# Optimization experiments

Measured on AMD Instinct MI355X. Metric: run time of the kernel, lower is better.

The kernel has to match this reference:

```python
import jax, jax.numpy as jnp
import numpy as np

B, N, C, H = 4, 2048, 256, 8
D = C // H  # head_dim = 32


def setup_inputs() -> dict:
    key = jax.random.key(0)
    ks = jax.random.split(key, 6)
    scale = 0.02
    return {
        "x": jax.random.normal(ks[0], (B, N, C), dtype=jnp.float32),
        # PPI interaction strengths in [0,1] (buffer, not trained)
        "interaction_mask": jax.random.uniform(ks[1], (N, N), dtype=jnp.float32),
        "W_qkv": jax.random.normal(ks[2], (C, 3 * C), dtype=jnp.float32) * scale,
        "b_qkv": jnp.zeros((3 * C,), dtype=jnp.float32),
        "W_out": jax.random.normal(ks[3], (C, C), dtype=jnp.float32) * scale,
        "b_out": jnp.zeros((C,), dtype=jnp.float32),
    }


def reference(x, interaction_mask, W_qkv, b_qkv, W_out, b_out):
    Bb, Nn, Cc = x.shape
    scale = D ** -0.5
    qkv = (x @ W_qkv + b_qkv).reshape(Bb, Nn, 3, H, D)
    qkv = jnp.transpose(qkv, (2, 0, 3, 1, 4))  # [3, B, H, N, D]
    q, k, v = qkv[0], qkv[1], qkv[2]
    # scores [B, H, N, N], modulated pre-softmax by biological mask
    attn = jnp.einsum("bhnd,bhmd->bhnm", q, k) * scale
    attn = attn * (0.1 + 0.9 * interaction_mask)[None, None, :, :]
    attn = jax.nn.softmax(attn, axis=-1)  # dropout is identity in eval
    out = jnp.einsum("bhnm,bhmd->bhnd", attn, v)
    out = jnp.transpose(out, (0, 2, 1, 3)).reshape(Bb, Nn, Cc)
    return out @ W_out + b_out
```

## Files before the change

kernel.cpp:

```cpp
#include <hip/hip_runtime.h>
#include <hip/hip_bf16.h>

#define B_ 4
#define N_ 2048
#define C_ 256
#define H_ 8
#define D_ 32

typedef __attribute__((ext_vector_type(4))) short bf16x4;
typedef __attribute__((ext_vector_type(8))) short bf16x8;
typedef __attribute__((ext_vector_type(16))) float f32x16;

static __device__ __forceinline__ float b2f(short u) {
    unsigned v = ((unsigned)(unsigned short)u) << 16;
    return __builtin_bit_cast(float, v);
}
static __device__ __forceinline__ short f2bs(float f) {
    __hip_bfloat16 h = __float2bfloat16(f);
    return __builtin_bit_cast(short, h);
}


__global__ __launch_bounds__(256) void x_relayout(const float* __restrict__ x,
                                                  short* __restrict__ xF) {
    const int idx = blockIdx.x * 256 + threadIdx.x;
    const int row = idx >> 6, c0 = (idx & 63) * 4;
    const float4 f4 = *(const float4*)(x + (size_t)row * 256 + c0);
    const int mt = row >> 5, l5 = row & 31;
    const int kt = c0 >> 5, dd0 = c0 & 31;
    const int hi = (dd0 >> 2) & 1, s0 = 4 * (dd0 >> 3);
    bf16x4 o;
    o[0] = f2bs(f4.x); o[1] = f2bs(f4.y); o[2] = f2bs(f4.z); o[3] = f2bs(f4.w);
    *(bf16x4*)(xF + (((size_t)mt * 8 + kt) * 32 + l5) * 32 + hi * 16 + s0) = o;
}

__global__ __launch_bounds__(256) void w_relayout(const float* __restrict__ Wq,
                                                  const float* __restrict__ Wo,
                                                  short* __restrict__ wqF,
                                                  short* __restrict__ woF) {
    int idx = blockIdx.x * 256 + threadIdx.x;
    const float* W; short* dst; int ncols;
    if (idx < 49152) { W = Wq; dst = wqF; ncols = 768; }
    else { idx -= 49152; W = Wo; dst = woF; ncols = 256; }
    const int f4pr = ncols >> 2;
    const int row = idx / f4pr, c0 = (idx % f4pr) * 4;
    const float4 f4 = *(const float4*)(W + (size_t)row * ncols + c0);
    const int kt = row >> 5, dd = row & 31;
    const int hi = (dd >> 2) & 1, s = (dd & 3) + 4 * (dd >> 3);
    const float vals[4] = {f4.x, f4.y, f4.z, f4.w};
#pragma unroll
    for (int j = 0; j < 4; ++j) {
        const int col = c0 + j, nt = col >> 5, l5 = col & 31;
        dst[(((size_t)nt * 8 + kt) * 32 + l5) * 32 + hi * 16 + s] = f2bs(vals[j]);
    }
}

__global__ __launch_bounds__(256) void mask_relayout(const float* __restrict__ mask,
                                                     short* __restrict__ maskF) {
    const int t = threadIdx.x;
    const int n = blockIdx.y * 64 + (t & 63);
    const int mt = blockIdx.x * 4 + (t >> 6);
    const float cf = 0.17677669529663687f * 1.4426950408889634f;
    float v[32];
    const float4* src = (const float4*)(mask + (size_t)n * N_ + mt * 32);
#pragma unroll
    for (int i = 0; i < 8; ++i) {
        const float4 f4 = src[i];
        v[i * 4 + 0] = f4.x; v[i * 4 + 1] = f4.y;
        v[i * 4 + 2] = f4.z; v[i * 4 + 3] = f4.w;
    }
#pragma unroll
    for (int hi = 0; hi < 2; ++hi) {
        bf16x8 o0, o1;
#pragma unroll
        for (int r = 0; r < 16; ++r) {
            const int crow = (r & 3) + 8 * (r >> 2) + 4 * hi;
            const short s = f2bs(cf * (0.1f + 0.9f * v[crow]));
            if (r < 8) o0[r] = s; else o1[r - 8] = s;
        }
        short* dst = maskF + ((size_t)(mt * 2 + hi) * N_ + n) * 16;
        *(bf16x8*)dst = o0;
        *(bf16x8*)(dst + 8) = o1;
    }
}

__global__ __launch_bounds__(256, 4) void qkv_mfma(const short* __restrict__ xF,
                                                   const short* __restrict__ wqF,
                                                   const float* __restrict__ bias,
                                                   short* __restrict__ qb,
                                                   short* __restrict__ kbF,
                                                   short* __restrict__ vbF) {
    __shared__ short sc[4][32 * 34];
    const int t = threadIdx.x;
    const int w = t >> 6, lane = t & 63, l5 = lane & 31, hi = lane >> 5;
    const int tile = blockIdx.x * 4 + w;
    const int nt = tile % 24, mt = tile / 24;
    f32x16 acc;
#pragma unroll
    for (int i = 0; i < 16; ++i) acc[i] = 0.f;
    const short* ap = xF + ((size_t)mt * 8 * 32) * 32 + l5 * 32 + hi * 16;
    const short* bp = wqF + ((size_t)nt * 8 * 32) * 32 + l5 * 32 + hi * 16;
#pragma unroll
    for (int kt = 0; kt < 8; ++kt) {
        const bf16x8 a0 = *(const bf16x8*)(ap + kt * 1024);
        const bf16x8 a1 = *(const bf16x8*)(ap + kt * 1024 + 8);
        const bf16x8 b0 = *(const bf16x8*)(bp + kt * 1024);
        const bf16x8 b1 = *(const bf16x8*)(bp + kt * 1024 + 8);
        acc = __builtin_amdgcn_mfma_f32_32x32x16_bf16(a0, b0, acc, 0, 0, 0);
        acc = __builtin_amdgcn_mfma_f32_32x32x16_bf16(a1, b1, acc, 0, 0, 0);
    }
    const float bq = bias[nt * 32 + l5];
    short* myc = sc[w];
#pragma unroll
    for (int r = 0; r < 16; ++r)
        myc[((r & 3) + 8 * (r >> 2) + 4 * hi) * 34 + l5] = f2bs(acc[r] + bq);
    __syncthreads();

    const int h = nt & 7, t3 = nt >> 3;
    const int mtk = mt & 63;
    const size_t bh = (size_t)(mt >> 6) * 8 + h;
    if (t3 == 0) {
        const bf16x8 r0 = *(const bf16x8*)(myc + l5 * 34 + hi * 16);
        const bf16x8 r1 = *(const bf16x8*)(myc + l5 * 34 + hi * 16 + 8);
        short* dst = qb + (bh * N_ + (size_t)mtk * 32 + l5) * D_ + hi * 16;
        *(bf16x8*)dst = r0;
        *(bf16x8*)(dst + 8) = r1;
    } else if (t3 == 1) {
        bf16x8 o0, o1;
#pragma unroll
        for (int s = 0; s < 16; ++s) {
            const int dd = hi * 4 + (s & 3) + 8 * (s >> 2);
            const short vv = myc[l5 * 34 + dd];
            if (s < 8) o0[s] = vv; else o1[s - 8] = vv;
        }
        short* dst = kbF + ((bh * 64 + mtk) * 32 + l5) * 32 + hi * 16;
        *(bf16x8*)dst = o0;
        *(bf16x8*)(dst + 8) = o1;
    } else {
        bf16x8 o0, o1;
#pragma unroll
        for (int s = 0; s < 16; ++s) {
            const int nl = hi * 4 + (s & 3) + 8 * (s >> 2);
            const short vv = myc[nl * 34 + l5];
            if (s < 8) o0[s] = vv; else o1[s - 8] = vv;
        }
        short* dst = vbF + ((bh * 64 + mtk) * 32 + l5) * 32 + hi * 16;
        *(bf16x8*)dst = o0;
        *(bf16x8*)(dst + 8) = o1;
    }
}

__global__ __launch_bounds__(256, 4) void attn_mfma(const short* __restrict__ qb,
                                                    const short* __restrict__ kbF,
                                                    const short* __restrict__ vbF,
                                                    const short* __restrict__ maskF,
                                                    short* __restrict__ aoF) {
    __shared__ float red[4][32][33];
    __shared__ float Ls[4][32];
    const int t = threadIdx.x;
    const int w = t >> 6, lane = t & 63, l5 = lane & 31, hi = lane >> 5;
    const int hi4 = hi * 4;
    const int bh = blockIdx.x >> 5, qg = blockIdx.x & 31;
    const int q0 = qg * 64;
    const int nqA = q0 + l5, nqB = q0 + 32 + l5;

    const short* qrA = qb + ((size_t)bh * N_ + nqA) * D_;
    const short* qrB = qb + ((size_t)bh * N_ + nqB) * D_;
    const bf16x8 qfA0 = __builtin_shufflevector(*(const bf16x4*)(qrA + hi4),
                                                *(const bf16x4*)(qrA + hi4 + 8),
                                                0, 1, 2, 3, 4, 5, 6, 7);
    const bf16x8 qfA1 = __builtin_shufflevector(*(const bf16x4*)(qrA + hi4 + 16),
                                                *(const bf16x4*)(qrA + hi4 + 24),
                                                0, 1, 2, 3, 4, 5, 6, 7);
    const bf16x8 qfB0 = __builtin_shufflevector(*(const bf16x4*)(qrB + hi4),
                                                *(const bf16x4*)(qrB + hi4 + 8),
                                                0, 1, 2, 3, 4, 5, 6, 7);
    const bf16x8 qfB1 = __builtin_shufflevector(*(const bf16x4*)(qrB + hi4 + 16),
                                                *(const bf16x4*)(qrB + hi4 + 24),
                                                0, 1, 2, 3, 4, 5, 6, 7);
    f32x16 accA, accB;
#pragma unroll
    for (int i = 0; i < 16; ++i) { accA[i] = 0.f; accB[i] = 0.f; }
    float lsA = 0.f, lsB = 0.f;

    const size_t fragbase = (size_t)bh * 64 * 1024;
#pragma unroll 4
    for (int i = 0; i < 16; ++i) {
        const int mt = w * 16 + i;
        const short* kp = kbF + fragbase + (size_t)mt * 1024 + l5 * 32 + hi * 16;
        const bf16x8 af0 = *(const bf16x8*)kp;
        const bf16x8 af1 = *(const bf16x8*)(kp + 8);
        f32x16 sA, sB;
#pragma unroll
        for (int j = 0; j < 16; ++j) { sA[j] = 0.f; sB[j] = 0.f; }
        sA = __builtin_amdgcn_mfma_f32_32x32x16_bf16(af0, qfA0, sA, 0, 0, 0);
        sA = __builtin_amdgcn_mfma_f32_32x32x16_bf16(af1, qfA1, sA, 0, 0, 0);
        sB = __builtin_amdgcn_mfma_f32_32x32x16_bf16(af0, qfB0, sB, 0, 0, 0);
        sB = __builtin_amdgcn_mfma_f32_32x32x16_bf16(af1, qfB1, sB, 0, 0, 0);

        const short* mpA = maskF + ((size_t)(mt * 2 + hi) * N_ + nqA) * 16;
        const short* mpB = maskF + ((size_t)(mt * 2 + hi) * N_ + nqB) * 16;
        const bf16x8 mA0 = *(const bf16x8*)mpA;
        const bf16x8 mA1 = *(const bf16x8*)(mpA + 8);
        const bf16x8 mB0 = *(const bf16x8*)mpB;
        const bf16x8 mB1 = *(const bf16x8*)(mpB + 8);

        bf16x8 pfA0, pfA1, pfB0, pfB1;
#pragma unroll
        for (int r = 0; r < 16; ++r) {
            const float fmA = b2f(r < 8 ? mA0[r] : mA1[r - 8]);
            const float fmB = b2f(r < 8 ? mB0[r] : mB1[r - 8]);
            const float pA = __builtin_amdgcn_exp2f(sA[r] * fmA);
            const float pB = __builtin_amdgcn_exp2f(sB[r] * fmB);
            lsA += pA; lsB += pB;
            const short hA = f2bs(pA), hB = f2bs(pB);
            if (r < 8) { pfA0[r] = hA; pfB0[r] = hB; }
            else       { pfA1[r - 8] = hA; pfB1[r - 8] = hB; }
        }
        const short* vp = vbF + fragbase + (size_t)mt * 1024 + l5 * 32 + hi * 16;
        const bf16x8 vf0 = *(const bf16x8*)vp;
        const bf16x8 vf1 = *(const bf16x8*)(vp + 8);
        accA = __builtin_amdgcn_mfma_f32_32x32x16_bf16(vf0, pfA0, accA, 0, 0, 0);
        accA = __builtin_amdgcn_mfma_f32_32x32x16_bf16(vf1, pfA1, accA, 0, 0, 0);
        accB = __builtin_amdgcn_mfma_f32_32x32x16_bf16(vf0, pfB0, accB, 0, 0, 0);
        accB = __builtin_amdgcn_mfma_f32_32x32x16_bf16(vf1, pfB1, accB, 0, 0, 0);
    }

    const int h = bh & 7;
    const int gmtb = (bh >> 3) * 64 + qg * 2;
#pragma unroll
    for (int tq = 0; tq < 2; ++tq) {
        if (tq) __syncthreads();
        const float lsum = tq ? lsB : lsA;
        const f32x16 acc = tq ? accB : accA;
        const float lt = lsum + __shfl_xor(lsum, 32);
        Ls[w][l5] = lt;
#pragma unroll
        for (int r = 0; r < 16; ++r)
            red[w][(r & 3) + 8 * (r >> 2) + hi4][l5] = acc[r];
        __syncthreads();
        const int row = t & 31, hi2 = (t >> 5) & 1, sh = t >> 6;
        const float inv = 1.0f / (Ls[0][row] + Ls[1][row] + Ls[2][row] + Ls[3][row]);
        bf16x4 o;
#pragma unroll
        for (int j = 0; j < 4; ++j) {
            const int dd = hi2 * 4 + j + 8 * sh;
            o[j] = f2bs((red[0][dd][row] + red[1][dd][row] +
                         red[2][dd][row] + red[3][dd][row]) * inv);
        }
        const size_t gmt = gmtb + tq;
        *(bf16x4*)(aoF + ((gmt * 8 + h) * 32 + row) * 32 + hi2 * 16 + sh * 4) = o;
    }
}

__global__ __launch_bounds__(256, 4) void out_mfma(const short* __restrict__ aoF,
                                                   const short* __restrict__ woF,
                                                   const float* __restrict__ bias,
                                                   float* __restrict__ out) {
    const int t = threadIdx.x;
    const int w = t >> 6, lane = t & 63, l5 = lane & 31, hi = lane >> 5;
    const int tile = blockIdx.x * 4 + w;
    const int nt = tile & 7, mt = tile >> 3;
    f32x16 acc;
#pragma unroll
    for (int i = 0; i < 16; ++i) acc[i] = 0.f;
    const short* ap = aoF + (size_t)mt * 8192 + l5 * 32 + hi * 16;
    const short* bp = woF + (size_t)nt * 8192 + l5 * 32 + hi * 16;
#pragma unroll
    for (int kt = 0; kt < 8; ++kt) {
        const bf16x8 a0 = *(const bf16x8*)(ap + kt * 1024);
        const bf16x8 a1 = *(const bf16x8*)(ap + kt * 1024 + 8);
        const bf16x8 b0 = *(const bf16x8*)(bp + kt * 1024);
        const bf16x8 b1 = *(const bf16x8*)(bp + kt * 1024 + 8);
        acc = __builtin_amdgcn_mfma_f32_32x32x16_bf16(a0, b0, acc, 0, 0, 0);
        acc = __builtin_amdgcn_mfma_f32_32x32x16_bf16(a1, b1, acc, 0, 0, 0);
    }
    const float bo = bias[nt * 32 + l5];
#pragma unroll
    for (int r = 0; r < 16; ++r) {
        const int crow = (r & 3) + 8 * (r >> 2) + 4 * hi;
        out[(size_t)(mt * 32 + crow) * 256 + nt * 32 + l5] = acc[r] + bo;
    }
}

extern "C" void kernel_launch(void* const* d_in, const int* in_sizes, int n_in,
                              void* d_out, int out_size, void* d_ws, size_t ws_size,
                              hipStream_t stream) {
    const float* x = (const float*)d_in[0];
    const float* mask = (const float*)d_in[1];
    const float* W_qkv = (const float*)d_in[2];
    const float* b_qkv = (const float*)d_in[3];
    const float* W_out = (const float*)d_in[4];
    const float* b_out = (const float*)d_in[5];
    float* out = (float*)d_out;

    const size_t per = (size_t)B_ * H_ * N_ * D_;
    short* qb = (short*)d_ws;
    short* kbF = qb + per;
    short* vbF = kbF + per;
    short* maskF = vbF + per;
    short* xF = maskF + (size_t)N_ * N_;
    short* wqF = xF + per;
    short* woF = wqF + 196608;
    short* aoF = xF;

    x_relayout<<<2048, 256, 0, stream>>>(x, xF);
    w_relayout<<<256, 256, 0, stream>>>(W_qkv, W_out, wqF, woF);
    mask_relayout<<<dim3(16, 32), 256, 0, stream>>>(mask, maskF);
    qkv_mfma<<<1536, 256, 0, stream>>>(xF, wqF, b_qkv, qb, kbF, vbF);
    attn_mfma<<<1024, 256, 0, stream>>>(qb, kbF, vbF, maskF, aoF);
    out_mfma<<<512, 256, 0, stream>>>(aoF, woF, b_out, out);
}
```

Measured before the change: 79.48 us.

## Merge relayout kernels, split MFMA accumulators, reorder attention loads, remap blocks

```diff
diff --git a/kernel.cpp b/kernel.cpp
--- a/kernel.cpp
+++ b/kernel.cpp
@@ -21,66 +21,69 @@
 }
 
 
-__global__ __launch_bounds__(256) void x_relayout(const float* __restrict__ x,
-                                                  short* __restrict__ xF) {
-    const int idx = blockIdx.x * 256 + threadIdx.x;
-    const int row = idx >> 6, c0 = (idx & 63) * 4;
-    const float4 f4 = *(const float4*)(x + (size_t)row * 256 + c0);
-    const int mt = row >> 5, l5 = row & 31;
-    const int kt = c0 >> 5, dd0 = c0 & 31;
-    const int hi = (dd0 >> 2) & 1, s0 = 4 * (dd0 >> 3);
-    bf16x4 o;
-    o[0] = f2bs(f4.x); o[1] = f2bs(f4.y); o[2] = f2bs(f4.z); o[3] = f2bs(f4.w);
-    *(bf16x4*)(xF + (((size_t)mt * 8 + kt) * 32 + l5) * 32 + hi * 16 + s0) = o;
-}
-
-__global__ __launch_bounds__(256) void w_relayout(const float* __restrict__ Wq,
-                                                  const float* __restrict__ Wo,
-                                                  short* __restrict__ wqF,
-                                                  short* __restrict__ woF) {
-    int idx = blockIdx.x * 256 + threadIdx.x;
-    const float* W; short* dst; int ncols;
-    if (idx < 49152) { W = Wq; dst = wqF; ncols = 768; }
-    else { idx -= 49152; W = Wo; dst = woF; ncols = 256; }
-    const int f4pr = ncols >> 2;
-    const int row = idx / f4pr, c0 = (idx % f4pr) * 4;
-    const float4 f4 = *(const float4*)(W + (size_t)row * ncols + c0);
-    const int kt = row >> 5, dd = row & 31;
-    const int hi = (dd >> 2) & 1, s = (dd & 3) + 4 * (dd >> 3);
-    const float vals[4] = {f4.x, f4.y, f4.z, f4.w};
-#pragma unroll
-    for (int j = 0; j < 4; ++j) {
-        const int col = c0 + j, nt = col >> 5, l5 = col & 31;
-        dst[(((size_t)nt * 8 + kt) * 32 + l5) * 32 + hi * 16 + s] = f2bs(vals[j]);
-    }
-}
-
-__global__ __launch_bounds__(256) void mask_relayout(const float* __restrict__ mask,
+__global__ __launch_bounds__(256) void prep_relayout(const float* __restrict__ x,
+                                                     const float* __restrict__ Wq,
+                                                     const float* __restrict__ Wo,
+                                                     const float* __restrict__ mask,
+                                                     short* __restrict__ xF,
+                                                     short* __restrict__ wqF,
+                                                     short* __restrict__ woF,
                                                      short* __restrict__ maskF) {
     const int t = threadIdx.x;
-    const int n = blockIdx.y * 64 + (t & 63);
-    const int mt = blockIdx.x * 4 + (t >> 6);
-    const float cf = 0.17677669529663687f * 1.4426950408889634f;
-    float v[32];
-    const float4* src = (const float4*)(mask + (size_t)n * N_ + mt * 32);
-#pragma unroll
-    for (int i = 0; i < 8; ++i) {
-        const float4 f4 = src[i];
-        v[i * 4 + 0] = f4.x; v[i * 4 + 1] = f4.y;
-        v[i * 4 + 2] = f4.z; v[i * 4 + 3] = f4.w;
-    }
-#pragma unroll
-    for (int hi = 0; hi < 2; ++hi) {
-        bf16x8 o0, o1;
-#pragma unroll
-        for (int r = 0; r < 16; ++r) {
-            const int crow = (r & 3) + 8 * (r >> 2) + 4 * hi;
-            const short s = f2bs(cf * (0.1f + 0.9f * v[crow]));
-            if (r < 8) o0[r] = s; else o1[r - 8] = s;
-        }
-        short* dst = maskF + ((size_t)(mt * 2 + hi) * N_ + n) * 16;
-        *(bf16x8*)dst = o0;
-        *(bf16x8*)(dst + 8) = o1;
+    const int b = blockIdx.x;
+    if (b < 2048) {
+        const int idx = b * 256 + t;
+        const int row = idx >> 6, c0 = (idx & 63) * 4;
+        const float4 f4 = *(const float4*)(x + (size_t)row * 256 + c0);
+        const int mt = row >> 5, l5 = row & 31;
+        const int kt = c0 >> 5, dd0 = c0 & 31;
+        const int hi = (dd0 >> 2) & 1, s0 = 4 * (dd0 >> 3);
+        bf16x4 o;
+        o[0] = f2bs(f4.x); o[1] = f2bs(f4.y); o[2] = f2bs(f4.z); o[3] = f2bs(f4.w);
+        *(bf16x4*)(xF + (((size_t)mt * 8 + kt) * 32 + l5) * 32 + hi * 16 + s0) = o;
+    } else if (b < 2304) {
+        int idx = (b - 2048) * 256 + t;
+        const float* W; short* dst; int ncols;
+        if (idx < 49152) { W = Wq; dst = wqF; ncols = 768; }
+        else { idx -= 49152; W = Wo; dst = woF; ncols = 256; }
+        const int f4pr = ncols >> 2;
+        const int row = idx / f4pr, c0 = (idx % f4pr) * 4;
+        const float4 f4 = *(const float4*)(W + (size_t)row * ncols + c0);
+        const int kt = row >> 5, dd = row & 31;
+        const int hi = (dd >> 2) & 1, s = (dd & 3) + 4 * (dd >> 3);
+        const float vals[4] = {f4.x, f4.y, f4.z, f4.w};
+#pragma unroll
+        for (int j = 0; j < 4; ++j) {
+            const int col = c0 + j, nt = col >> 5, l5 = col & 31;
+            dst[(((size_t)nt * 8 + kt) * 32 + l5) * 32 + hi * 16 + s] = f2bs(vals[j]);
+        }
+    } else {
+        const int bid = b - 2304;
+        const int bx = bid & 15, by = bid >> 4;
+        const int n = by * 64 + (t & 63);
+        const int mt = bx * 4 + (t >> 6);
+        const float cf = 0.17677669529663687f * 1.4426950408889634f;
+        float v[32];
+        const float4* src = (const float4*)(mask + (size_t)n * N_ + mt * 32);
+#pragma unroll
+        for (int i = 0; i < 8; ++i) {
+            const float4 f4 = src[i];
+            v[i * 4 + 0] = f4.x; v[i * 4 + 1] = f4.y;
+            v[i * 4 + 2] = f4.z; v[i * 4 + 3] = f4.w;
+        }
+#pragma unroll
+        for (int hi = 0; hi < 2; ++hi) {
+            bf16x8 o0, o1;
+#pragma unroll
+            for (int r = 0; r < 16; ++r) {
+                const int crow = (r & 3) + 8 * (r >> 2) + 4 * hi;
+                const short s = f2bs(cf * (0.1f + 0.9f * v[crow]));
+                if (r < 8) o0[r] = s; else o1[r - 8] = s;
+            }
+            short* dst = maskF + ((size_t)(mt * 2 + hi) * N_ + n) * 16;
+            *(bf16x8*)dst = o0;
+            *(bf16x8*)(dst + 8) = o1;
+        }
     }
 }
 
@@ -95,25 +98,32 @@
     const int w = t >> 6, lane = t & 63, l5 = lane & 31, hi = lane >> 5;
     const int tile = blockIdx.x * 4 + w;
     const int nt = tile % 24, mt = tile / 24;
-    f32x16 acc;
-#pragma unroll
-    for (int i = 0; i < 16; ++i) acc[i] = 0.f;
+    f32x16 acc0, acc1;
+#pragma unroll
+    for (int i = 0; i < 16; ++i) { acc0[i] = 0.f; acc1[i] = 0.f; }
     const short* ap = xF + ((size_t)mt * 8 * 32) * 32 + l5 * 32 + hi * 16;
     const short* bp = wqF + ((size_t)nt * 8 * 32) * 32 + l5 * 32 + hi * 16;
 #pragma unroll
-    for (int kt = 0; kt < 8; ++kt) {
+    for (int kt = 0; kt < 8; kt += 2) {
         const bf16x8 a0 = *(const bf16x8*)(ap + kt * 1024);
         const bf16x8 a1 = *(const bf16x8*)(ap + kt * 1024 + 8);
         const bf16x8 b0 = *(const bf16x8*)(bp + kt * 1024);
         const bf16x8 b1 = *(const bf16x8*)(bp + kt * 1024 + 8);
-        acc = __builtin_amdgcn_mfma_f32_32x32x16_bf16(a0, b0, acc, 0, 0, 0);
-        acc = __builtin_amdgcn_mfma_f32_32x32x16_bf16(a1, b1, acc, 0, 0, 0);
+        const bf16x8 a2 = *(const bf16x8*)(ap + kt * 1024 + 1024);
+        const bf16x8 a3 = *(const bf16x8*)(ap + kt * 1024 + 1032);
+        const bf16x8 b2 = *(const bf16x8*)(bp + kt * 1024 + 1024);
+        const bf16x8 b3 = *(const bf16x8*)(bp + kt * 1024 + 1032);
+        acc0 = __builtin_amdgcn_mfma_f32_32x32x16_bf16(a0, b0, acc0, 0, 0, 0);
+        acc1 = __builtin_amdgcn_mfma_f32_32x32x16_bf16(a2, b2, acc1, 0, 0, 0);
+        acc0 = __builtin_amdgcn_mfma_f32_32x32x16_bf16(a1, b1, acc0, 0, 0, 0);
+        acc1 = __builtin_amdgcn_mfma_f32_32x32x16_bf16(a3, b3, acc1, 0, 0, 0);
     }
     const float bq = bias[nt * 32 + l5];
     short* myc = sc[w];
 #pragma unroll
     for (int r = 0; r < 16; ++r)
-        myc[((r & 3) + 8 * (r >> 2) + 4 * hi) * 34 + l5] = f2bs(acc[r] + bq);
+        myc[((r & 3) + 8 * (r >> 2) + 4 * hi) * 34 + l5] =
+            f2bs(acc0[r] + acc1[r] + bq);
     __syncthreads();
 
     const int h = nt & 7, t3 = nt >> 3;
@@ -160,7 +170,8 @@
     const int t = threadIdx.x;
     const int w = t >> 6, lane = t & 63, l5 = lane & 31, hi = lane >> 5;
     const int hi4 = hi * 4;
-    const int bh = blockIdx.x >> 5, qg = blockIdx.x & 31;
+    const int vb = (blockIdx.x & 7) * 128 + (blockIdx.x >> 3);
+    const int bh = vb >> 5, qg = vb & 31;
     const int q0 = qg * 64;
     const int nqA = q0 + l5, nqB = q0 + 32 + l5;
 
@@ -181,29 +192,34 @@
     f32x16 accA, accB;
 #pragma unroll
     for (int i = 0; i < 16; ++i) { accA[i] = 0.f; accB[i] = 0.f; }
-    float lsA = 0.f, lsB = 0.f;
+    float lsA0 = 0.f, lsA1 = 0.f, lsB0 = 0.f, lsB1 = 0.f;
 
     const size_t fragbase = (size_t)bh * 64 * 1024;
 #pragma unroll 4
     for (int i = 0; i < 16; ++i) {
         const int mt = w * 16 + i;
-        const short* kp = kbF + fragbase + (size_t)mt * 1024 + l5 * 32 + hi * 16;
-        const bf16x8 af0 = *(const bf16x8*)kp;
-        const bf16x8 af1 = *(const bf16x8*)(kp + 8);
-        f32x16 sA, sB;
-#pragma unroll
-        for (int j = 0; j < 16; ++j) { sA[j] = 0.f; sB[j] = 0.f; }
-        sA = __builtin_amdgcn_mfma_f32_32x32x16_bf16(af0, qfA0, sA, 0, 0, 0);
-        sA = __builtin_amdgcn_mfma_f32_32x32x16_bf16(af1, qfA1, sA, 0, 0, 0);
-        sB = __builtin_amdgcn_mfma_f32_32x32x16_bf16(af0, qfB0, sB, 0, 0, 0);
-        sB = __builtin_amdgcn_mfma_f32_32x32x16_bf16(af1, qfB1, sB, 0, 0, 0);
-
         const short* mpA = maskF + ((size_t)(mt * 2 + hi) * N_ + nqA) * 16;
         const short* mpB = maskF + ((size_t)(mt * 2 + hi) * N_ + nqB) * 16;
         const bf16x8 mA0 = *(const bf16x8*)mpA;
         const bf16x8 mA1 = *(const bf16x8*)(mpA + 8);
         const bf16x8 mB0 = *(const bf16x8*)mpB;
         const bf16x8 mB1 = *(const bf16x8*)(mpB + 8);
+        const short* vp = vbF + fragbase + (size_t)mt * 1024 + l5 * 32 + hi * 16;
+        const bf16x8 vf0 = *(const bf16x8*)vp;
+        const bf16x8 vf1 = *(const bf16x8*)(vp + 8);
+
+        const short* kp = kbF + fragbase + (size_t)mt * 1024 + l5 * 32 + hi * 16;
+        const bf16x8 af0 = *(const bf16x8*)kp;
+        const bf16x8 af1 = *(const bf16x8*)(kp + 8);
+        f32x16 sA, sB;
+#pragma unroll
+        for (int j = 0; j < 16; ++j) { sA[j] = 0.f; sB[j] = 0.f; }
+        __builtin_amdgcn_s_setprio(1);
+        sA = __builtin_amdgcn_mfma_f32_32x32x16_bf16(af0, qfA0, sA, 0, 0, 0);
+        sB = __builtin_amdgcn_mfma_f32_32x32x16_bf16(af0, qfB0, sB, 0, 0, 0);
+        sA = __builtin_amdgcn_mfma_f32_32x32x16_bf16(af1, qfA1, sA, 0, 0, 0);
+        sB = __builtin_amdgcn_mfma_f32_32x32x16_bf16(af1, qfB1, sB, 0, 0, 0);
+        __builtin_amdgcn_s_setprio(0);
 
         bf16x8 pfA0, pfA1, pfB0, pfB1;
 #pragma unroll
@@ -212,19 +228,20 @@
             const float fmB = b2f(r < 8 ? mB0[r] : mB1[r - 8]);
             const float pA = __builtin_amdgcn_exp2f(sA[r] * fmA);
             const float pB = __builtin_amdgcn_exp2f(sB[r] * fmB);
-            lsA += pA; lsB += pB;
+            if (r < 8) { lsA0 += pA; lsB0 += pB; }
+            else       { lsA1 += pA; lsB1 += pB; }
             const short hA = f2bs(pA), hB = f2bs(pB);
             if (r < 8) { pfA0[r] = hA; pfB0[r] = hB; }
             else       { pfA1[r - 8] = hA; pfB1[r - 8] = hB; }
         }
-        const short* vp = vbF + fragbase + (size_t)mt * 1024 + l5 * 32 + hi * 16;
-        const bf16x8 vf0 = *(const bf16x8*)vp;
-        const bf16x8 vf1 = *(const bf16x8*)(vp + 8);
+        __builtin_amdgcn_s_setprio(1);
         accA = __builtin_amdgcn_mfma_f32_32x32x16_bf16(vf0, pfA0, accA, 0, 0, 0);
+        accB = __builtin_amdgcn_mfma_f32_32x32x16_bf16(vf0, pfB0, accB, 0, 0, 0);
         accA = __builtin_amdgcn_mfma_f32_32x32x16_bf16(vf1, pfA1, accA, 0, 0, 0);
-        accB = __builtin_amdgcn_mfma_f32_32x32x16_bf16(vf0, pfB0, accB, 0, 0, 0);
         accB = __builtin_amdgcn_mfma_f32_32x32x16_bf16(vf1, pfB1, accB, 0, 0, 0);
-    }
+        __builtin_amdgcn_s_setprio(0);
+    }
+    const float lsA = lsA0 + lsA1, lsB = lsB0 + lsB1;
 
     const int h = bh & 7;
     const int gmtb = (bh >> 3) * 64 + qg * 2;
@@ -261,25 +278,32 @@
     const int w = t >> 6, lane = t & 63, l5 = lane & 31, hi = lane >> 5;
     const int tile = blockIdx.x * 4 + w;
     const int nt = tile & 7, mt = tile >> 3;
-    f32x16 acc;
-#pragma unroll
-    for (int i = 0; i < 16; ++i) acc[i] = 0.f;
+    f32x16 acc0, acc1;
+#pragma unroll
+    for (int i = 0; i < 16; ++i) { acc0[i] = 0.f; acc1[i] = 0.f; }
     const short* ap = aoF + (size_t)mt * 8192 + l5 * 32 + hi * 16;
     const short* bp = woF + (size_t)nt * 8192 + l5 * 32 + hi * 16;
 #pragma unroll
-    for (int kt = 0; kt < 8; ++kt) {
+    for (int kt = 0; kt < 8; kt += 2) {
         const bf16x8 a0 = *(const bf16x8*)(ap + kt * 1024);
         const bf16x8 a1 = *(const bf16x8*)(ap + kt * 1024 + 8);
         const bf16x8 b0 = *(const bf16x8*)(bp + kt * 1024);
         const bf16x8 b1 = *(const bf16x8*)(bp + kt * 1024 + 8);
-        acc = __builtin_amdgcn_mfma_f32_32x32x16_bf16(a0, b0, acc, 0, 0, 0);
-        acc = __builtin_amdgcn_mfma_f32_32x32x16_bf16(a1, b1, acc, 0, 0, 0);
+        const bf16x8 a2 = *(const bf16x8*)(ap + kt * 1024 + 1024);
+        const bf16x8 a3 = *(const bf16x8*)(ap + kt * 1024 + 1032);
+        const bf16x8 b2 = *(const bf16x8*)(bp + kt * 1024 + 1024);
+        const bf16x8 b3 = *(const bf16x8*)(bp + kt * 1024 + 1032);
+        acc0 = __builtin_amdgcn_mfma_f32_32x32x16_bf16(a0, b0, acc0, 0, 0, 0);
+        acc1 = __builtin_amdgcn_mfma_f32_32x32x16_bf16(a2, b2, acc1, 0, 0, 0);
+        acc0 = __builtin_amdgcn_mfma_f32_32x32x16_bf16(a1, b1, acc0, 0, 0, 0);
+        acc1 = __builtin_amdgcn_mfma_f32_32x32x16_bf16(a3, b3, acc1, 0, 0, 0);
     }
     const float bo = bias[nt * 32 + l5];
 #pragma unroll
     for (int r = 0; r < 16; ++r) {
         const int crow = (r & 3) + 8 * (r >> 2) + 4 * hi;
-        out[(size_t)(mt * 32 + crow) * 256 + nt * 32 + l5] = acc[r] + bo;
+        out[(size_t)(mt * 32 + crow) * 256 + nt * 32 + l5] =
+            acc0[r] + acc1[r] + bo;
     }
 }
 
@@ -304,9 +328,8 @@
     short* woF = wqF + 196608;
     short* aoF = xF;
 
-    x_relayout<<<2048, 256, 0, stream>>>(x, xF);
-    w_relayout<<<256, 256, 0, stream>>>(W_qkv, W_out, wqF, woF);
-    mask_relayout<<<dim3(16, 32), 256, 0, stream>>>(mask, maskF);
+    prep_relayout<<<2816, 256, 0, stream>>>(x, W_qkv, W_out, mask,
+                                            xF, wqF, woF, maskF);
     qkv_mfma<<<1536, 256, 0, stream>>>(xF, wqF, b_qkv, qb, kbF, vbF);
     attn_mfma<<<1024, 256, 0, stream>>>(qb, kbF, vbF, maskF, aoF);
     out_mfma<<<512, 256, 0, stream>>>(aoF, woF, b_out, out);
```

Measured after the change: 83.20 us. 4.7% more time.
